# Performance work log

Measured on AMD Instinct MI355X. Metric: run time of the kernel, lower is better.

The kernel has to match this reference:

```python
import jax, jax.numpy as jnp
import numpy as np


def setup_inputs() -> dict:
    key = jax.random.key(0)
    ks = jax.random.split(key, 8)
    B = 32768
    return {
        "x": jax.random.normal(ks[0], (B, 784), dtype=jnp.float32),
        "conv_w": jax.random.normal(ks[1], (3, 3), dtype=jnp.float32),
        "fc1_w": jax.random.normal(ks[2], (512, 676), dtype=jnp.float32) * 0.04,
        "fc1_b": jax.random.normal(ks[3], (512,), dtype=jnp.float32),
        "fc2_w": jax.random.normal(ks[4], (512, 512), dtype=jnp.float32) * 0.04,
        "fc2_b": jax.random.normal(ks[5], (512,), dtype=jnp.float32),
        "out_w": jax.random.normal(ks[6], (10, 512), dtype=jnp.float32) * 0.04,
        "out_b": jax.random.normal(ks[7], (10,), dtype=jnp.float32),
    }


def reference(x, conv_w, fc1_w, fc1_b, fc2_w, fc2_b, out_w, out_b):
    B = x.shape[0]
    img = x.reshape(B, 1, 28, 28)  # NCHW, single channel
    # Valid 3x3 cross-correlation (same math as the nested tensordot loop).
    kern = conv_w.reshape(1, 1, 3, 3)  # OIHW
    conv = jax.lax.conv_general_dilated(
        img, kern, window_strides=(1, 1), padding="VALID",
        dimension_numbers=("NCHW", "OIHW", "NCHW"))  # [B,1,26,26]
    h = conv.reshape(B, 26 * 26)
    h = jax.nn.relu(h @ fc1_w.T + fc1_b)
    h = jax.nn.relu(h @ fc2_w.T + fc2_b)
    return h @ out_w.T + out_b  # [B,10] logits
```

## Files before the change

kernel.cpp:

```cpp
#include <hip/hip_runtime.h>

typedef unsigned short ushort_t;
typedef __attribute__((ext_vector_type(8))) short bf16x8;
typedef __attribute__((ext_vector_type(4))) float f32x4;
typedef __attribute__((ext_vector_type(16))) float f32x16;

__device__ __forceinline__ unsigned short f2bf(float f) {
    union { float f; unsigned u; } v; v.f = f;
    unsigned r = v.u + 0x7FFFu + ((v.u >> 16) & 1u);
    return (unsigned short)(r >> 16);
}

__device__ __forceinline__ unsigned cvt_pk_bf16(float a, float b) {
    unsigned r;
    asm("v_cvt_pk_bf16_f32 %0, %1, %2" : "=v"(r) : "v"(a), "v"(b));
    return r;
}

__global__ __launch_bounds__(256) void prep_w(const float* __restrict__ fc1_w,
                                              const float* __restrict__ cw,
                                              const float* __restrict__ fc2_w,
                                              const float* __restrict__ out_w,
                                              ushort_t* __restrict__ W1,
                                              ushort_t* __restrict__ W2,
                                              ushort_t* __restrict__ W3) {
    const int idx = blockIdx.x * 256 + threadIdx.x;
    if (idx < 425984) {
        const int ngrp = idx / 26624;
        const int kfrag = (idx % 26624) >> 9;
        const int li = idx & 511;
        const int lane = li >> 3, e = li & 7;
        const int n = ngrp * 32 + (lane & 31);
        const int p = kfrag * 16 + (lane >> 5) * 8 + e;
        float acc = 0.f;
        if (p < 784) {
            const int pr = p / 28, pc = p % 28;
            const float* frow = &fc1_w[n * 676];
#pragma unroll
            for (int dr = 0; dr < 3; ++dr) {
                const int r = pr - dr;
                const bool rok = (unsigned)r < 26u;
                const int rc = rok ? r : 0;
#pragma unroll
                for (int dc = 0; dc < 3; ++dc) {
                    const int c = pc - dc;
                    const bool cok = (unsigned)c < 26u;
                    const int cc = cok ? c : 0;
                    const float w = (rok && cok) ? cw[dr * 3 + dc] : 0.f;
                    acc += w * frow[rc * 26 + cc];
                }
            }
        }
        W1[idx] = f2bf(acc);
    }
    if (idx < 262144) {
        const int ngrp = idx / 16384;
        const int kfrag = (idx % 16384) >> 9;
        const int li = idx & 511;
        const int lane = li >> 3, e = li & 7;
        const int n = ngrp * 32 + (lane & 31);
        const int p = kfrag * 16 + (lane >> 5) * 8 + e;
        W2[idx] = f2bf(fc2_w[n * 512 + p]);
    }
    if (idx < 16 * 512)  W3[idx] = (idx < 10 * 512) ? f2bf(out_w[idx]) : (ushort_t)0;
}

__global__ __launch_bounds__(512, 4) void mega13(const float* __restrict__ x,
                                                 const ushort_t* __restrict__ W1,
                                                 const ushort_t* __restrict__ W2,
                                                 const ushort_t* __restrict__ W3,
                                                 const float* __restrict__ b1,
                                                 const float* __restrict__ b2,
                                                 const float* __restrict__ ob,
                                                 float* __restrict__ out) {
    extern __shared__ ushort_t smem[];
    ushort_t* xs0 = smem;
    ushort_t* hs  = smem + 4096;

    const int tid = threadIdx.x;
    const int wave = tid >> 6, lane = tid & 63;
    const int r32 = lane & 31, khalf = lane >> 5;
    const int xrow = tid >> 3, xoct = tid & 7;
    const int m0 = blockIdx.x * 64;
    const size_t ng0 = wave * 2, ng1 = wave * 2 + 1;

    const ushort_t* w1p0 = &W1[ng0 * 52 * 512 + lane * 8];
    const ushort_t* w1p1 = &W1[ng1 * 52 * 512 + lane * 8];
    const ushort_t* w2p0 = &W2[ng0 * 32 * 512 + lane * 8];
    const ushort_t* w2p1 = &W2[ng1 * 32 * 512 + lane * 8];

    f32x16 acc[2][2];
#pragma unroll
    for (int a = 0; a < 2; ++a)
#pragma unroll
        for (int j = 0; j < 2; ++j)
#pragma unroll
            for (int e = 0; e < 16; ++e) acc[a][j][e] = 0.f;

    f32x4 xv0, xv1;
    auto load_x = [&](int ks) {
        const int gc = ks * 64 + xoct * 8;
        if (gc < 784) {
            const f32x4* p = (const f32x4*)&x[(size_t)(m0 + xrow) * 784 + gc];
            xv0 = __builtin_nontemporal_load(p);
            xv1 = __builtin_nontemporal_load(p + 1);
        } else {
            xv0 = (f32x4){0.f, 0.f, 0.f, 0.f};
            xv1 = (f32x4){0.f, 0.f, 0.f, 0.f};
        }
    };
    auto store_x = [&](ushort_t* buf) {
        union { bf16x8 h; unsigned u[4]; } a, b;
        a.u[0] = cvt_pk_bf16(xv0.x, xv0.y); a.u[1] = cvt_pk_bf16(xv0.z, xv0.w);
        a.u[2] = cvt_pk_bf16(xv1.x, xv1.y); a.u[3] = cvt_pk_bf16(xv1.z, xv1.w);
        (void)b;
        *(bf16x8*)&buf[xrow * 64 + ((xoct ^ (xrow & 7)) * 8)] = a.h;
    };

    auto write_h = [&](const float* __restrict__ bias) {
#pragma unroll
        for (int j = 0; j < 2; ++j) {
            const int n = (wave * 2 + j) * 32 + r32;
            const float bb = bias[n];
            const int nseg = n >> 3, nrem = n & 7;
#pragma unroll
            for (int i = 0; i < 2; ++i)
#pragma unroll
                for (int reg = 0; reg < 16; ++reg) {
                    const int m = i * 32 + 4 * khalf + (reg & 3) + 8 * (reg >> 2);
                    hs[m * 512 + ((nseg ^ (m & 7)) * 8) + nrem] = f2bf(fmaxf(acc[i][j][reg] + bb, 0.f));
                }
        }
    };

    load_x(0);
    store_x(xs0);
    __syncthreads();

    bf16x8 bwc0 = *(const bf16x8*)(w1p0);
    bf16x8 bwc1 = *(const bf16x8*)(w1p1);

    for (int ks = 0; ks < 12; ++ks) {
        load_x(ks + 1);
        const ushort_t* bufp = (ks & 1) ? hs : xs0;
#pragma unroll
        for (int ksub = 0; ksub < 4; ++ksub) {
            const int kf = ks * 4 + ksub;
            bf16x8 bwn0, bwn1;
            if (kf < 48) {
                bwn0 = *(const bf16x8*)(w1p0 + (kf + 1) * 512);
                bwn1 = *(const bf16x8*)(w1p1 + (kf + 1) * 512);
            } else {
                bwn0 = *(const bf16x8*)(w2p0);
                bwn1 = *(const bf16x8*)(w2p1);
            }
            const int q = 2 * ksub + khalf;
            bf16x8 af[2];
#pragma unroll
            for (int i = 0; i < 2; ++i) {
                const int m = i * 32 + r32;
                af[i] = *(const bf16x8*)&bufp[m * 64 + ((q ^ (m & 7)) * 8)];
            }
            __builtin_amdgcn_s_setprio(1);
            acc[0][0] = __builtin_amdgcn_mfma_f32_32x32x16_bf16(af[0], bwc0, acc[0][0], 0, 0, 0);
            acc[0][1] = __builtin_amdgcn_mfma_f32_32x32x16_bf16(af[0], bwc1, acc[0][1], 0, 0, 0);
            acc[1][0] = __builtin_amdgcn_mfma_f32_32x32x16_bf16(af[1], bwc0, acc[1][0], 0, 0, 0);
            acc[1][1] = __builtin_amdgcn_mfma_f32_32x32x16_bf16(af[1], bwc1, acc[1][1], 0, 0, 0);
            __builtin_amdgcn_s_setprio(0);
            bwc0 = bwn0; bwc1 = bwn1;
        }
        store_x((ks & 1) ? xs0 : hs);
        __syncthreads();
    }
    {
        const ushort_t* bufp = xs0;
        bf16x8 bwn0 = *(const bf16x8*)(w2p0);
        bf16x8 bwn1 = *(const bf16x8*)(w2p1);
        const int q = khalf;
        bf16x8 af[2];
#pragma unroll
        for (int i = 0; i < 2; ++i) {
            const int m = i * 32 + r32;
            af[i] = *(const bf16x8*)&bufp[m * 64 + ((q ^ (m & 7)) * 8)];
        }
        __builtin_amdgcn_s_setprio(1);
        acc[0][0] = __builtin_amdgcn_mfma_f32_32x32x16_bf16(af[0], bwc0, acc[0][0], 0, 0, 0);
        acc[0][1] = __builtin_amdgcn_mfma_f32_32x32x16_bf16(af[0], bwc1, acc[0][1], 0, 0, 0);
        acc[1][0] = __builtin_amdgcn_mfma_f32_32x32x16_bf16(af[1], bwc0, acc[1][0], 0, 0, 0);
        acc[1][1] = __builtin_amdgcn_mfma_f32_32x32x16_bf16(af[1], bwc1, acc[1][1], 0, 0, 0);
        __builtin_amdgcn_s_setprio(0);
        bwc0 = bwn0; bwc1 = bwn1;
    }

    write_h(b1);
#pragma unroll
    for (int a = 0; a < 2; ++a)
#pragma unroll
        for (int j = 0; j < 2; ++j)
#pragma unroll
            for (int e = 0; e < 16; ++e) acc[a][j][e] = 0.f;
    __syncthreads();

    for (int ks = 0; ks < 8; ++ks) {
#pragma unroll
        for (int ksub = 0; ksub < 4; ++ksub) {
            const int kf = ks * 4 + ksub;
            bf16x8 bwn0, bwn1;
            if (kf < 31) {
                bwn0 = *(const bf16x8*)(w2p0 + (kf + 1) * 512);
                bwn1 = *(const bf16x8*)(w2p1 + (kf + 1) * 512);
            }
            const int hq = kf * 2 + khalf;
            bf16x8 af[2];
#pragma unroll
            for (int i = 0; i < 2; ++i) {
                const int m = i * 32 + r32;
                af[i] = *(const bf16x8*)&hs[m * 512 + ((hq ^ (m & 7)) * 8)];
            }
            __builtin_amdgcn_s_setprio(1);
            acc[0][0] = __builtin_amdgcn_mfma_f32_32x32x16_bf16(af[0], bwc0, acc[0][0], 0, 0, 0);
            acc[0][1] = __builtin_amdgcn_mfma_f32_32x32x16_bf16(af[0], bwc1, acc[0][1], 0, 0, 0);
            acc[1][0] = __builtin_amdgcn_mfma_f32_32x32x16_bf16(af[1], bwc0, acc[1][0], 0, 0, 0);
            acc[1][1] = __builtin_amdgcn_mfma_f32_32x32x16_bf16(af[1], bwc1, acc[1][1], 0, 0, 0);
            __builtin_amdgcn_s_setprio(0);
            if (kf < 31) { bwc0 = bwn0; bwc1 = bwn1; }
        }
    }
    __syncthreads();

    write_h(b2);
    __syncthreads();

    if (wave < 4) {
        const int quad = lane >> 4, l16 = lane & 15;
        const int row = wave * 16 + l16;
        f32x4 hacc = {0.f, 0.f, 0.f, 0.f};
#pragma unroll
        for (int ks = 0; ks < 16; ++ks) {
            const int seg = 4 * ks + quad;
            const bf16x8 a = *(const bf16x8*)&hs[row * 512 + ((seg ^ (row & 7)) * 8)];
            const bf16x8 b = *(const bf16x8*)&W3[l16 * 512 + ks * 32 + quad * 8];
            hacc = __builtin_amdgcn_mfma_f32_16x16x32_bf16(a, b, hacc, 0, 0, 0);
        }
        if (l16 < 10) {
            const float bb = ob[l16];
#pragma unroll
            for (int r = 0; r < 4; ++r)
                out[(size_t)(m0 + wave * 16 + quad * 4 + r) * 10 + l16] = hacc[r] + bb;
        }
    }
}

extern "C" void kernel_launch(void* const* d_in, const int* in_sizes, int n_in,
                              void* d_out, int out_size, void* d_ws, size_t ws_size,
                              hipStream_t stream) {
    const float* x      = (const float*)d_in[0];
    const float* conv_w = (const float*)d_in[1];
    const float* fc1_w  = (const float*)d_in[2];
    const float* fc1_b  = (const float*)d_in[3];
    const float* fc2_w  = (const float*)d_in[4];
    const float* fc2_b  = (const float*)d_in[5];
    const float* out_w  = (const float*)d_in[6];
    const float* out_b  = (const float*)d_in[7];
    float* out = (float*)d_out;

    ushort_t* W1 = (ushort_t*)d_ws;
    ushort_t* W2 = W1 + 425984;
    ushort_t* W3 = W2 + 262144;

    prep_w<<<dim3(1664), 256, 0, stream>>>(fc1_w, conv_w, fc2_w, out_w, W1, W2, W3);

    mega13<<<dim3(512), 512, 73728, stream>>>(x, W1, W2, W3, fc1_b, fc2_b, out_b, out);
}
```

Baseline: 214.8 us.

## Restructure weight prep kernel with padded LDS staging and vectorized conversions

The prep kernel now has one wave per fc1 output row. Each wave stages the 26x26 weights into a zero-padded 30x30 LDS tile, so the conv-folded W1 entries are computed without bounds checks or repeated global gathers. W2 conversion is vectorized to four elements per thread and W3 is handled by a single block, which cuts the grid from 1664 to 385 blocks. This lowers the preprocessing cost that runs before the main fused kernel, at the price of scattered W1 writes and fewer, heavier blocks.

```diff
diff --git a/kernel.cpp b/kernel.cpp
--- a/kernel.cpp
+++ b/kernel.cpp
@@ -3,6 +3,7 @@
 typedef unsigned short ushort_t;
 typedef __attribute__((ext_vector_type(8))) short bf16x8;
 typedef __attribute__((ext_vector_type(4))) float f32x4;
+typedef __attribute__((ext_vector_type(4))) unsigned short u16x4;
 typedef __attribute__((ext_vector_type(16))) float f32x16;
 
 __device__ __forceinline__ unsigned short f2bf(float f) {
@@ -24,45 +25,60 @@
                                               ushort_t* __restrict__ W1,
                                               ushort_t* __restrict__ W2,
                                               ushort_t* __restrict__ W3) {
-    const int idx = blockIdx.x * 256 + threadIdx.x;
-    if (idx < 425984) {
-        const int ngrp = idx / 26624;
-        const int kfrag = (idx % 26624) >> 9;
-        const int li = idx & 511;
-        const int lane = li >> 3, e = li & 7;
+    __shared__ float Fp[4][900];
+    const int tid = threadIdx.x, bid = blockIdx.x;
+    if (bid < 128) {
+        const int wid = tid >> 6, lane = tid & 63;
+        const int n = bid * 4 + wid;
+        float* F = Fp[wid];
+#pragma unroll
+        for (int t = 0; t < 15; ++t) {
+            const int i = t * 64 + lane;
+            if (i < 900) F[i] = 0.f;
+        }
+        __syncthreads();
+#pragma unroll
+        for (int t = 0; t < 11; ++t) {
+            const int i = t * 64 + lane;
+            if (i < 676) {
+                const int r = i / 26, c = i - r * 26;
+                F[(r + 2) * 30 + (c + 2)] = fc1_w[n * 676 + i];
+            }
+        }
+        __syncthreads();
+        const float k00 = cw[0], k01 = cw[1], k02 = cw[2];
+        const float k10 = cw[3], k11 = cw[4], k12 = cw[5];
+        const float k20 = cw[6], k21 = cw[7], k22 = cw[8];
+        const int ngrp = n >> 5, r32n = n & 31;
+#pragma unroll
+        for (int t = 0; t < 13; ++t) {
+            const int p = t * 64 + lane;
+            float v = 0.f;
+            if (p < 784) {
+                const int pr = p / 28, pc = p - pr * 28;
+                const int rb = (pr + 2) * 30 + (pc + 2);
+                v = k00 * F[rb]      + k01 * F[rb - 1]  + k02 * F[rb - 2]
+                  + k10 * F[rb - 30] + k11 * F[rb - 31] + k12 * F[rb - 32]
+                  + k20 * F[rb - 60] + k21 * F[rb - 61] + k22 * F[rb - 62];
+            }
+            W1[(ngrp * 52 + (p >> 4)) * 512 + (((p >> 3) & 1) * 32 + r32n) * 8 + (p & 7)] = f2bf(v);
+        }
+    } else if (bid < 384) {
+        const int base = (bid - 128) * 1024 + tid * 4;
+        const int ngrp = base >> 14;
+        const int kfrag = (base >> 9) & 31;
+        const int li = base & 511;
+        const int lane = li >> 3;
         const int n = ngrp * 32 + (lane & 31);
-        const int p = kfrag * 16 + (lane >> 5) * 8 + e;
-        float acc = 0.f;
-        if (p < 784) {
-            const int pr = p / 28, pc = p % 28;
-            const float* frow = &fc1_w[n * 676];
-#pragma unroll
-            for (int dr = 0; dr < 3; ++dr) {
-                const int r = pr - dr;
-                const bool rok = (unsigned)r < 26u;
-                const int rc = rok ? r : 0;
-#pragma unroll
-                for (int dc = 0; dc < 3; ++dc) {
-                    const int c = pc - dc;
-                    const bool cok = (unsigned)c < 26u;
-                    const int cc = cok ? c : 0;
-                    const float w = (rok && cok) ? cw[dr * 3 + dc] : 0.f;
-                    acc += w * frow[rc * 26 + cc];
-                }
-            }
-        }
-        W1[idx] = f2bf(acc);
-    }
-    if (idx < 262144) {
-        const int ngrp = idx / 16384;
-        const int kfrag = (idx % 16384) >> 9;
-        const int li = idx & 511;
-        const int lane = li >> 3, e = li & 7;
-        const int n = ngrp * 32 + (lane & 31);
-        const int p = kfrag * 16 + (lane >> 5) * 8 + e;
-        W2[idx] = f2bf(fc2_w[n * 512 + p]);
-    }
-    if (idx < 16 * 512)  W3[idx] = (idx < 10 * 512) ? f2bf(out_w[idx]) : (ushort_t)0;
+        const int p0 = kfrag * 16 + (lane >> 5) * 8 + (li & 7);
+        const f32x4 v = *(const f32x4*)&fc2_w[n * 512 + p0];
+        u16x4 o;
+        o[0] = f2bf(v.x); o[1] = f2bf(v.y); o[2] = f2bf(v.z); o[3] = f2bf(v.w);
+        *(u16x4*)&W2[base] = o;
+    } else {
+        for (int idx = tid; idx < 8192; idx += 256)
+            W3[idx] = (idx < 5120) ? f2bf(out_w[idx]) : (ushort_t)0;
+    }
 }
 
 __global__ __launch_bounds__(512, 4) void mega13(const float* __restrict__ x,
@@ -110,10 +126,9 @@
         }
     };
     auto store_x = [&](ushort_t* buf) {
-        union { bf16x8 h; unsigned u[4]; } a, b;
+        union { bf16x8 h; unsigned u[4]; } a;
         a.u[0] = cvt_pk_bf16(xv0.x, xv0.y); a.u[1] = cvt_pk_bf16(xv0.z, xv0.w);
         a.u[2] = cvt_pk_bf16(xv1.x, xv1.y); a.u[3] = cvt_pk_bf16(xv1.z, xv1.w);
-        (void)b;
         *(bf16x8*)&buf[xrow * 64 + ((xoct ^ (xrow & 7)) * 8)] = a.h;
     };
 
@@ -268,7 +283,7 @@
     ushort_t* W2 = W1 + 425984;
     ushort_t* W3 = W2 + 262144;
 
-    prep_w<<<dim3(1664), 256, 0, stream>>>(fc1_w, conv_w, fc2_w, out_w, W1, W2, W3);
+    prep_w<<<dim3(385), 256, 0, stream>>>(fc1_w, conv_w, fc2_w, out_w, W1, W2, W3);
 
     mega13<<<dim3(512), 512, 73728, stream>>>(x, W1, W2, W3, fc1_b, fc2_b, out_b, out);
 }
```

New measurement: 220.8 us. 1.03x slower.
